# Performance work log

Hardware: AMD Instinct MI355X
Metric: run time of the kernel (lower is better)

## Reference

```python
import jax, jax.numpy as jnp
import numpy as np

INPUT_SIZE = 1024
HIDDEN_SIZE = 1024
N_LAYERS = 2
OUTPUT_SIZE = 4096
BATCH = 4096


def setup_inputs() -> dict:
    key = jax.random.key(0)
    ks = jax.random.split(key, 12)
    s = 1.0 / np.sqrt(HIDDEN_SIZE)
    u = lambda k, shp: jax.random.uniform(k, shp, jnp.float32, -s, s)
    return {
        "input": jax.random.normal(ks[0], (1, BATCH, INPUT_SIZE), jnp.float32),
        "hidden": jax.random.normal(ks[1], (N_LAYERS, BATCH, HIDDEN_SIZE), jnp.float32),
        # nn.RNN layer 0 params
        "W_ih0": u(ks[2], (HIDDEN_SIZE, INPUT_SIZE)),
        "W_hh0": u(ks[3], (HIDDEN_SIZE, HIDDEN_SIZE)),
        "b_ih0": u(ks[4], (HIDDEN_SIZE,)),
        "b_hh0": u(ks[5], (HIDDEN_SIZE,)),
        # nn.RNN layer 1 params (input is layer-0 hidden)
        "W_ih1": u(ks[6], (HIDDEN_SIZE, HIDDEN_SIZE)),
        "W_hh1": u(ks[7], (HIDDEN_SIZE, HIDDEN_SIZE)),
        "b_ih1": u(ks[8], (HIDDEN_SIZE,)),
        "b_hh1": u(ks[9], (HIDDEN_SIZE,)),
        # i2o Linear(input_size + hidden_size, output_size)
        "W_out": u(ks[10], (OUTPUT_SIZE, INPUT_SIZE + HIDDEN_SIZE)),
        "b_out": u(ks[11], (OUTPUT_SIZE,)),
    }


def reference(input, hidden, W_ih0, W_hh0, b_ih0, b_hh0,
              W_ih1, W_hh1, b_ih1, b_hh1, W_out, b_out):
    x = input[0]  # [B, input_size] (seq_len == 1)
    # nn.RNN single step, tanh nonlinearity, 2 layers
    h0 = jnp.tanh(x @ W_ih0.T + b_ih0 + hidden[0] @ W_hh0.T + b_hh0)   # [B, H]
    h1 = jnp.tanh(h0 @ W_ih1.T + b_ih1 + hidden[1] @ W_hh1.T + b_hh1)  # [B, H]
    new_hidden = jnp.stack([h0, h1], axis=0)  # [n_layers, B, H]
    # combined = cat(input[0], hidden[0]) where hidden is the NEW hidden
    combined = jnp.concatenate([x, h0], axis=1)  # [B, input+hidden]
    logits = combined @ W_out.T + b_out          # [B, output_size]
    out = jax.nn.log_softmax(logits, axis=1)
    return (out, new_hidden)
```

## Files before the change

kernel.cpp:

```cpp
#include <hip/hip_runtime.h>
#include <math.h>


typedef __attribute__((ext_vector_type(8))) short bf16x8;
typedef __attribute__((ext_vector_type(4))) float f32x4;

__device__ __forceinline__ unsigned short f2b_rne(float f) {
    unsigned int x = __float_as_uint(f);
    x += 0x7FFF + ((x >> 16) & 1);
    return (unsigned short)(x >> 16);
}

__device__ __forceinline__ void gload_lds16(const void* g, void* l) {
    __builtin_amdgcn_global_load_lds(
        (const __attribute__((address_space(1))) void*)g,
        (__attribute__((address_space(3))) void*)l,
        16, 0, 0);
}

struct CvtSeg { const float* src; unsigned short* dst; unsigned n8; };
struct CvtArgs { CvtSeg seg[8]; };

__global__ __launch_bounds__(256) void f2b_multi(CvtArgs a)
{
    unsigned i = blockIdx.x * 256u + threadIdx.x;
#pragma unroll
    for (int s = 0; s < 8; ++s) {
        if (i < a.seg[s].n8) {
            const float4* src = (const float4*)a.seg[s].src;
            float4 u = src[2 * (size_t)i];
            float4 v = src[2 * (size_t)i + 1];
            unsigned short t[8] = {
                f2b_rne(u.x), f2b_rne(u.y), f2b_rne(u.z), f2b_rne(u.w),
                f2b_rne(v.x), f2b_rne(v.y), f2b_rne(v.z), f2b_rne(v.w)};
            *(uint4*)(a.seg[s].dst + 8 * (size_t)i) = *(const uint4*)t;
            return;
        }
        i -= a.seg[s].n8;
    }
}

struct GemmP {
    const unsigned short *Aa, *Ab; int lda;
    const unsigned short *Wa, *Wb; int ldw;
    const float *ba, *bb;
    float* C; int ldc;
    unsigned short* Cb; int ldcb;
    int nx, nb, do_tanh;
};

template<int BM, int BN>
__device__ __forceinline__ void gemm2p_body(
    const GemmP& p, int bid0, unsigned short* As, unsigned short* Ws, int tid)
{
    constexpr int FM = BM / 32;
    constexpr int FN = BN / 32;
    int bid = (bid0 & 7) * (p.nb >> 3) + (bid0 >> 3);
    const int row0 = (bid / p.nx) * BM;
    const int col0 = (bid % p.nx) * BN;

    const int wid = tid >> 6, lane = tid & 63;
    const int wr = wid >> 1, wc = wid & 1;
    const int fr = lane & 15, fk = lane >> 4;

    f32x4 acc[FM][FN] = {};

    for (int h = 0; h < 2; ++h) {
        const unsigned short* A = h ? p.Ab : p.Aa;
        const unsigned short* W = h ? p.Wb : p.Wa;
        for (int k0 = 0; k0 < 1024; k0 += 32) {
#pragma unroll
            for (int i = 0; i < BM / 64; ++i) {
                int c = i * 256 + wid * 64 + lane;
                int r = c >> 2, ol = c & 3;
                int os = ol ^ ((r >> 1) & 3);
                gload_lds16(A + (size_t)(row0 + r) * p.lda + k0 + os * 8,
                            As + (i * 256 + wid * 64) * 8);
            }
#pragma unroll
            for (int i = 0; i < BN / 64; ++i) {
                int c = i * 256 + wid * 64 + lane;
                int r = c >> 2, ol = c & 3;
                int os = ol ^ ((r >> 1) & 3);
                gload_lds16(W + (size_t)(col0 + r) * p.ldw + k0 + os * 8,
                            Ws + (i * 256 + wid * 64) * 8);
            }
            __syncthreads();

            bf16x8 af[FM], wf[FN];
#pragma unroll
            for (int m = 0; m < FM; ++m) {
                int r = wr * (BM / 2) + m * 16 + fr;
                af[m] = *(const bf16x8*)&As[r * 32 + ((fk ^ ((r >> 1) & 3)) * 8)];
            }
#pragma unroll
            for (int n = 0; n < FN; ++n) {
                int r = wc * (BN / 2) + n * 16 + fr;
                wf[n] = *(const bf16x8*)&Ws[r * 32 + ((fk ^ ((r >> 1) & 3)) * 8)];
            }
#pragma unroll
            for (int m = 0; m < FM; ++m)
#pragma unroll
                for (int n = 0; n < FN; ++n)
                    acc[m][n] = __builtin_amdgcn_mfma_f32_16x16x32_bf16(
                        af[m], wf[n], acc[m][n], 0, 0, 0);
            __syncthreads();
        }
    }

    const bool dot = p.do_tanh != 0;
#pragma unroll
    for (int n = 0; n < FN; ++n) {
        const int col = col0 + wc * (BN / 2) + n * 16 + fr;
        float b = p.ba[col];
        if (p.bb) b += p.bb[col];
#pragma unroll
        for (int m = 0; m < FM; ++m) {
#pragma unroll
            for (int j = 0; j < 4; ++j) {
                const int r = row0 + wr * (BM / 2) + m * 16 + fk * 4 + j;
                float v = acc[m][n][j] + b;
                if (dot) v = tanhf(v);
                p.C[(size_t)r * p.ldc + col] = v;
                if (p.Cb) p.Cb[(size_t)r * p.ldcb + col] = f2b_rne(v);
            }
        }
    }
}

__global__ __launch_bounds__(256) void gemm1_k(GemmP p)
{
    __shared__ __align__(16) unsigned short As[128 * 32];
    __shared__ __align__(16) unsigned short Ws[64 * 32];
    gemm2p_body<128, 64>(p, blockIdx.x, As, Ws, threadIdx.x);
}

__device__ __forceinline__ void logsoftmax_row(float* __restrict__ p, int tid)
{
    const int lane = tid & 63;
    const int wv = tid >> 6;
    __shared__ float redm[4];
    __shared__ float reds[4];

    float v[16];
#pragma unroll
    for (int i = 0; i < 16; ++i) v[i] = p[tid + i * 256];

    float m = v[0];
#pragma unroll
    for (int i = 1; i < 16; ++i) m = fmaxf(m, v[i]);
#pragma unroll
    for (int off = 32; off; off >>= 1) m = fmaxf(m, __shfl_xor(m, off));
    if (lane == 0) redm[wv] = m;
    __syncthreads();
    m = fmaxf(fmaxf(redm[0], redm[1]), fmaxf(redm[2], redm[3]));

    float s = 0.f;
#pragma unroll
    for (int i = 0; i < 16; ++i) s += expf(v[i] - m);
#pragma unroll
    for (int off = 32; off; off >>= 1) s += __shfl_xor(s, off);
    if (lane == 0) reds[wv] = s;
    __syncthreads();
    s = reds[0] + reds[1] + reds[2] + reds[3];

    const float lse = m + logf(s);
#pragma unroll
    for (int i = 0; i < 16; ++i) p[tid + i * 256] = v[i] - lse;
}

__global__ __launch_bounds__(256) void g2sm_k(GemmP p, float* __restrict__ logits)
{
    if (blockIdx.x < 512) {
        __shared__ __align__(16) unsigned short As[128 * 32];
        __shared__ __align__(16) unsigned short Ws[64 * 32];
        gemm2p_body<128, 64>(p, blockIdx.x, As, Ws, threadIdx.x);
    } else {
        logsoftmax_row(logits + (size_t)(blockIdx.x - 512) * 4096, threadIdx.x);
    }
}


__device__ __forceinline__ void stage_half8(
    const unsigned short* __restrict__ src, int ld, int base_rc, int tau, int h,
    unsigned short* lds, int wid, int lane, bool isA)
{
    unsigned short* dst = lds + (tau & 1) * 16384 + h * 8192 + wid * 1024;
    const int k0 = (tau & 15) << 6;
#pragma unroll
    for (int i = 0; i < 2; ++i) {
        int c = wid * 128 + i * 64 + lane;
        int ir = c >> 3, cc = c & 7;
        int grow = isA ? (base_rc + h * 64 + (ir & 63) + ((ir >> 6) << 7))
                       : (base_rc + h * 32 + (ir & 31) + ((ir >> 5) << 6));
        int gk = k0 + (((cc ^ ir) & 7) << 3);
        gload_lds16(src + (size_t)grow * ld + gk, dst + i * 512);
    }
}

__global__ __launch_bounds__(512, 2) void gemm8p(
    const unsigned short* __restrict__ Aa, const unsigned short* __restrict__ Ab,
    const unsigned short* __restrict__ Wa, const unsigned short* __restrict__ Wb,
    int lda, int ldw, const float* __restrict__ bias,
    float* __restrict__ C, int ldc, int nx)
{
    constexpr int NT = 32;
    __shared__ __align__(16) unsigned short smem[65536];
    unsigned short* As = smem;
    unsigned short* Bs = smem + 32768;

    int bid = blockIdx.x;
    bid = (bid & 7) * 32 + (bid >> 3);
    const int row0 = (bid / nx) * 256;
    const int col0 = (bid % nx) * 256;

    const int tid = threadIdx.x;
    const int wid = tid >> 6, lane = tid & 63;
    const int wr = wid >> 2, wc = wid & 3;
    const int fr = lane & 15, fk = lane >> 4;
    const int ch0 = fk ^ (fr & 7);
    const int ch1 = ch0 ^ 4;

#define STA8(tau, h) stage_half8(((tau) < 16 ? Aa : Ab), lda, row0, (tau), (h), As, wid, lane, true)
#define STB8(tau, h) stage_half8(((tau) < 16 ? Wa : Wb), ldw, col0, (tau), (h), Bs, wid, lane, false)

#define LDAF(QM) { const unsigned short* Ap_ = Abase + (QM) * 8192;           \
    _Pragma("unroll") for (int mf = 0; mf < 4; ++mf) {                        \
        int ia = wr * 64 + mf * 16 + fr;                                      \
        af[mf][0] = *(const bf16x8*)&Ap_[ia * 64 + ch0 * 8];                  \
        af[mf][1] = *(const bf16x8*)&Ap_[ia * 64 + ch1 * 8]; } }

#define LDWF(QN, WF) { const unsigned short* Bp_ = Bbase + (QN) * 8192;       \
    _Pragma("unroll") for (int nf = 0; nf < 2; ++nf) {                        \
        int ib = wc * 32 + nf * 16 + fr;                                      \
        WF[nf][0] = *(const bf16x8*)&Bp_[ib * 64 + ch0 * 8];                  \
        WF[nf][1] = *(const bf16x8*)&Bp_[ib * 64 + ch1 * 8]; } }

#define MMQ(QM, QN, WF) {                                                     \
    __builtin_amdgcn_s_setprio(1);                                            \
    _Pragma("unroll") for (int mf = 0; mf < 4; ++mf)                          \
    _Pragma("unroll") for (int nf = 0; nf < 2; ++nf) {                        \
        acc[QM][QN][mf][nf] = __builtin_amdgcn_mfma_f32_16x16x32_bf16(        \
            af[mf][0], WF[nf][0], acc[QM][QN][mf][nf], 0, 0, 0);              \
        acc[QM][QN][mf][nf] = __builtin_amdgcn_mfma_f32_16x16x32_bf16(        \
            af[mf][1], WF[nf][1], acc[QM][QN][mf][nf], 0, 0, 0); }            \
    __builtin_amdgcn_s_setprio(0); }

    f32x4 acc[2][2][4][2] = {};
    bf16x8 af[4][2], wfA[2][2], wfB[2][2];

    STA8(0, 0); STB8(0, 0); STB8(0, 1); STA8(0, 1);

    for (int t = 0; t < NT; ++t) {
        const unsigned short* Abase = As + (t & 1) * 16384;
        const unsigned short* Bbase = Bs + (t & 1) * 16384;
        const bool more = (t + 1 < NT);

        asm volatile("s_waitcnt vmcnt(4)" ::: "memory");
        __builtin_amdgcn_s_barrier();
        LDAF(0); LDWF(0, wfA);
        if (more) STA8(t + 1, 0);
        MMQ(0, 0, wfA);

        if (more) { asm volatile("s_waitcnt vmcnt(4)" ::: "memory"); }
        else      { asm volatile("s_waitcnt vmcnt(2)" ::: "memory"); }
        __builtin_amdgcn_s_barrier();
        LDWF(1, wfB);
        if (more) STB8(t + 1, 0);
        MMQ(0, 1, wfB);

        if (more) { asm volatile("s_waitcnt vmcnt(4)" ::: "memory"); }
        else      { asm volatile("s_waitcnt vmcnt(0)" ::: "memory"); }
        __builtin_amdgcn_s_barrier();
        LDAF(1);
        if (more) STB8(t + 1, 1);
        MMQ(1, 1, wfB);

        if (more) STA8(t + 1, 1);
        MMQ(1, 0, wfA);
    }
#undef MMQ
#undef LDAF
#undef LDWF
#undef STA8
#undef STB8

    float bv[2][2];
#pragma unroll
    for (int qn = 0; qn < 2; ++qn)
#pragma unroll
        for (int nf = 0; nf < 2; ++nf)
            bv[qn][nf] = bias[col0 + wc * 64 + qn * 32 + nf * 16 + fr];

    float* Ct = (float*)smem;
    __syncthreads();
#pragma unroll
    for (int qm = 0; qm < 2; ++qm) {
        if (qm) __syncthreads();
#pragma unroll
        for (int qn = 0; qn < 2; ++qn)
#pragma unroll
            for (int nf = 0; nf < 2; ++nf) {
                const int col = wc * 64 + qn * 32 + nf * 16 + fr;
#pragma unroll
                for (int mf = 0; mf < 4; ++mf)
#pragma unroll
                    for (int j = 0; j < 4; ++j) {
                        int lr = wr * 64 + mf * 16 + fk * 4 + j;
                        int pc = col ^ (((lr >> 2) & 3) << 4);
                        Ct[lr * 256 + pc] = acc[qm][qn][mf][nf][j] + bv[qn][nf];
                    }
            }
        __syncthreads();
#pragma unroll
        for (int k = 0; k < 16; ++k) {
            int idx = k * 512 + tid;
            int lrow = idx >> 6, c4 = idx & 63;
            int pc4 = (c4 * 4) ^ (((lrow >> 2) & 3) << 4);
            int grow = row0 + qm * 64 + (lrow & 63) + ((lrow >> 6) << 7);
            *(float4*)&C[(size_t)grow * ldc + col0 + c4 * 4] =
                *(const float4*)&Ct[lrow * 256 + pc4];
        }
    }
}

extern "C" void kernel_launch(void* const* d_in, const int* in_sizes, int n_in,
                              void* d_out, int out_size, void* d_ws, size_t ws_size,
                              hipStream_t stream)
{
    (void)in_sizes; (void)n_in; (void)out_size; (void)ws_size;

    const float* input  = (const float*)d_in[0];
    const float* hidden = (const float*)d_in[1];
    const float* b_ih0  = (const float*)d_in[4];
    const float* b_hh0  = (const float*)d_in[5];
    const float* b_ih1  = (const float*)d_in[8];
    const float* b_hh1  = (const float*)d_in[9];
    const float* b_out  = (const float*)d_in[11];

    float* out = (float*)d_out;
    float* h0  = out + (size_t)4096 * 4096;
    float* h1  = h0 + (size_t)4096 * 1024;

    unsigned short* xb    = (unsigned short*)d_ws;
    unsigned short* hidb  = xb    + (size_t)4096 * 1024;
    unsigned short* h0b   = hidb  + (size_t)2 * 4096 * 1024;
    unsigned short* Wih0b = h0b   + (size_t)4096 * 1024;
    unsigned short* Whh0b = Wih0b + (size_t)1024 * 1024;
    unsigned short* Wih1b = Whh0b + (size_t)1024 * 1024;
    unsigned short* Whh1b = Wih1b + (size_t)1024 * 1024;
    unsigned short* Woutb = Whh1b + (size_t)1024 * 1024;
    unsigned short* hid0b = hidb;
    unsigned short* hid1b = hidb + (size_t)4096 * 1024;

    CvtArgs ca;
    ca.seg[0] = { input,                 xb,    524288u };
    ca.seg[1] = { hidden,                hidb, 1048576u };
    ca.seg[2] = { (const float*)d_in[2], Wih0b, 131072u };
    ca.seg[3] = { (const float*)d_in[3], Whh0b, 131072u };
    ca.seg[4] = { (const float*)d_in[6], Wih1b, 131072u };
    ca.seg[5] = { (const float*)d_in[7], Whh1b, 131072u };
    ca.seg[6] = { (const float*)d_in[10],Woutb, 1048576u };
    ca.seg[7] = { nullptr, nullptr, 0u };
    hipLaunchKernelGGL(f2b_multi, dim3(12288), dim3(256), 0, stream, ca);

    GemmP p1;
    p1.Aa = xb;    p1.Ab = hid0b; p1.lda = 1024;
    p1.Wa = Wih0b; p1.Wb = Whh0b; p1.ldw = 1024;
    p1.ba = b_ih0; p1.bb = b_hh0;
    p1.C = h0; p1.ldc = 1024; p1.Cb = h0b; p1.ldcb = 1024;
    p1.nx = 16; p1.nb = 512; p1.do_tanh = 1;
    hipLaunchKernelGGL(gemm1_k, dim3(512), dim3(256), 0, stream, p1);

    hipLaunchKernelGGL(gemm8p, dim3(256), dim3(512), 0, stream,
                       xb, h0b, Woutb, Woutb + 1024, 1024, 2048,
                       b_out, out, 4096, 16);

    GemmP p2;
    p2.Aa = h0b;   p2.Ab = hid1b; p2.lda = 1024;
    p2.Wa = Wih1b; p2.Wb = Whh1b; p2.ldw = 1024;
    p2.ba = b_ih1; p2.bb = b_hh1;
    p2.C = h1; p2.ldc = 1024; p2.Cb = nullptr; p2.ldcb = 0;
    p2.nx = 16; p2.nb = 512; p2.do_tanh = 1;
    hipLaunchKernelGGL(g2sm_k, dim3(4608), dim3(256), 0, stream, p2, out);
}
```

Baseline: 170.5 us.

## Vectorize log-softmax row access and restructure GEMM barrier/waitcnt schedule

The log-softmax row routine now loads and stores with float4 instead of scalar strided accesses, so each thread touches contiguous 16-byte chunks. The 8-wave GEMM main loop gains extra barriers with lgkmcnt(0) waits after each LDS fragment read and global-to-LDS stage issue, ahead of the MFMA block. The waitcnt+barrier at the top of each iteration moves to the end, with a prologue barrier added. This aims to synchronize waves around the MFMA clusters, ping-pong style, so memory issue and math from different waves interleave. It also adds more barriers per iteration, which can cost stall time.

Measured after the change: 172.8 us. Within noise of the previous version (+1.3%).

```diff
diff --git a/kernel.cpp b/kernel.cpp
--- a/kernel.cpp
+++ b/kernel.cpp
@@ -142,13 +142,15 @@
     __shared__ float redm[4];
     __shared__ float reds[4];
 
-    float v[16];
-#pragma unroll
-    for (int i = 0; i < 16; ++i) v[i] = p[tid + i * 256];
-
-    float m = v[0];
-#pragma unroll
-    for (int i = 1; i < 16; ++i) m = fmaxf(m, v[i]);
+    float4 v[4];
+#pragma unroll
+    for (int i = 0; i < 4; ++i) v[i] = ((const float4*)p)[i * 256 + tid];
+
+    float m = v[0].x;
+#pragma unroll
+    for (int i = 0; i < 4; ++i) {
+        m = fmaxf(m, fmaxf(fmaxf(v[i].x, v[i].y), fmaxf(v[i].z, v[i].w)));
+    }
 #pragma unroll
     for (int off = 32; off; off >>= 1) m = fmaxf(m, __shfl_xor(m, off));
     if (lane == 0) redm[wv] = m;
@@ -157,7 +159,10 @@
 
     float s = 0.f;
 #pragma unroll
-    for (int i = 0; i < 16; ++i) s += expf(v[i] - m);
+    for (int i = 0; i < 4; ++i) {
+        s += expf(v[i].x - m); s += expf(v[i].y - m);
+        s += expf(v[i].z - m); s += expf(v[i].w - m);
+    }
 #pragma unroll
     for (int off = 32; off; off >>= 1) s += __shfl_xor(s, off);
     if (lane == 0) reds[wv] = s;
@@ -166,7 +171,12 @@
 
     const float lse = m + logf(s);
 #pragma unroll
-    for (int i = 0; i < 16; ++i) p[tid + i * 256] = v[i] - lse;
+    for (int i = 0; i < 4; ++i) {
+        float4 o;
+        o.x = v[i].x - lse; o.y = v[i].y - lse;
+        o.z = v[i].z - lse; o.w = v[i].w - lse;
+        ((float4*)p)[i * 256 + tid] = o;
+    }
 }
 
 __global__ __launch_bounds__(256) void g2sm_k(GemmP p, float* __restrict__ logits)
@@ -246,44 +256,54 @@
             af[mf][1], WF[nf][1], acc[QM][QN][mf][nf], 0, 0, 0); }            \
     __builtin_amdgcn_s_setprio(0); }
 
+#define BAR() __builtin_amdgcn_s_barrier()
+#define LGKM0() asm volatile("s_waitcnt lgkmcnt(0)" ::: "memory")
+
     f32x4 acc[2][2][4][2] = {};
     bf16x8 af[4][2], wfA[2][2], wfB[2][2];
 
     STA8(0, 0); STB8(0, 0); STB8(0, 1); STA8(0, 1);
+    asm volatile("s_waitcnt vmcnt(4)" ::: "memory");
+    BAR();
 
     for (int t = 0; t < NT; ++t) {
         const unsigned short* Abase = As + (t & 1) * 16384;
         const unsigned short* Bbase = Bs + (t & 1) * 16384;
         const bool more = (t + 1 < NT);
 
-        asm volatile("s_waitcnt vmcnt(4)" ::: "memory");
-        __builtin_amdgcn_s_barrier();
         LDAF(0); LDWF(0, wfA);
         if (more) STA8(t + 1, 0);
+        BAR(); LGKM0();
         MMQ(0, 0, wfA);
-
         if (more) { asm volatile("s_waitcnt vmcnt(4)" ::: "memory"); }
         else      { asm volatile("s_waitcnt vmcnt(2)" ::: "memory"); }
-        __builtin_amdgcn_s_barrier();
+        BAR();
+
         LDWF(1, wfB);
         if (more) STB8(t + 1, 0);
+        BAR(); LGKM0();
         MMQ(0, 1, wfB);
-
         if (more) { asm volatile("s_waitcnt vmcnt(4)" ::: "memory"); }
         else      { asm volatile("s_waitcnt vmcnt(0)" ::: "memory"); }
-        __builtin_amdgcn_s_barrier();
+        BAR();
+
         LDAF(1);
         if (more) STB8(t + 1, 1);
+        BAR(); LGKM0();
         MMQ(1, 1, wfB);
 
         if (more) STA8(t + 1, 1);
         MMQ(1, 0, wfA);
+        if (more) asm volatile("s_waitcnt vmcnt(4)" ::: "memory");
+        BAR();
     }
 #undef MMQ
 #undef LDAF
 #undef LDWF
 #undef STA8
 #undef STB8
+#undef BAR
+#undef LGKM0
 
     float bv[2][2];
 #pragma unroll
```

## Store intermediate logits as bf16 and vectorize log-softmax loads

Applied to the files above, without the earlier changes.

The output GEMM now writes its logits as bf16 into a workspace buffer instead of fp32 into the output. The log-softmax pass reads these bf16 values and writes the final fp32 result, which cuts the traffic of the logits round trip. The fallback fp32 log-softmax path is rewritten to use float4 loads and stores. Storing logits in bf16 lowers their precision before the softmax, and the new path only runs when the workspace is large enough.

New measurement: 170.7 us. Within noise of the previous version (+0.1%).

```diff
diff --git a/kernel.cpp b/kernel.cpp
--- a/kernel.cpp
+++ b/kernel.cpp
@@ -135,20 +135,21 @@
     gemm2p_body<128, 64>(p, blockIdx.x, As, Ws, threadIdx.x);
 }
 
-__device__ __forceinline__ void logsoftmax_row(float* __restrict__ p, int tid)
+__device__ __forceinline__ void logsoftmax_row_f32(float* __restrict__ p, int tid)
 {
     const int lane = tid & 63;
     const int wv = tid >> 6;
     __shared__ float redm[4];
     __shared__ float reds[4];
 
-    float v[16];
-#pragma unroll
-    for (int i = 0; i < 16; ++i) v[i] = p[tid + i * 256];
-
-    float m = v[0];
-#pragma unroll
-    for (int i = 1; i < 16; ++i) m = fmaxf(m, v[i]);
+    float4 v[4];
+#pragma unroll
+    for (int i = 0; i < 4; ++i) v[i] = ((const float4*)p)[i * 256 + tid];
+
+    float m = v[0].x;
+#pragma unroll
+    for (int i = 0; i < 4; ++i)
+        m = fmaxf(m, fmaxf(fmaxf(v[i].x, v[i].y), fmaxf(v[i].z, v[i].w)));
 #pragma unroll
     for (int off = 32; off; off >>= 1) m = fmaxf(m, __shfl_xor(m, off));
     if (lane == 0) redm[wv] = m;
@@ -157,7 +158,10 @@
 
     float s = 0.f;
 #pragma unroll
-    for (int i = 0; i < 16; ++i) s += expf(v[i] - m);
+    for (int i = 0; i < 4; ++i) {
+        s += expf(v[i].x - m); s += expf(v[i].y - m);
+        s += expf(v[i].z - m); s += expf(v[i].w - m);
+    }
 #pragma unroll
     for (int off = 32; off; off >>= 1) s += __shfl_xor(s, off);
     if (lane == 0) reds[wv] = s;
@@ -166,17 +170,79 @@
 
     const float lse = m + logf(s);
 #pragma unroll
-    for (int i = 0; i < 16; ++i) p[tid + i * 256] = v[i] - lse;
-}
-
-__global__ __launch_bounds__(256) void g2sm_k(GemmP p, float* __restrict__ logits)
+    for (int i = 0; i < 4; ++i) {
+        float4 o;
+        o.x = v[i].x - lse; o.y = v[i].y - lse;
+        o.z = v[i].z - lse; o.w = v[i].w - lse;
+        ((float4*)p)[i * 256 + tid] = o;
+    }
+}
+
+__device__ __forceinline__ void logsoftmax_row_b16(
+    const unsigned short* __restrict__ lb, float* __restrict__ op, int tid)
+{
+    const int lane = tid & 63;
+    const int wv = tid >> 6;
+    __shared__ float redm[4];
+    __shared__ float reds[4];
+
+    uint4 r[2];
+    r[0] = *(const uint4*)&lb[tid * 8];
+    r[1] = *(const uint4*)&lb[2048 + tid * 8];
+    float v[16];
+#pragma unroll
+    for (int h = 0; h < 2; ++h)
+#pragma unroll
+        for (int j = 0; j < 4; ++j) {
+            unsigned u = ((const unsigned*)&r[h])[j];
+            v[h * 8 + 2 * j]     = __uint_as_float(u << 16);
+            v[h * 8 + 2 * j + 1] = __uint_as_float(u & 0xFFFF0000u);
+        }
+
+    float m = v[0];
+#pragma unroll
+    for (int i = 1; i < 16; ++i) m = fmaxf(m, v[i]);
+#pragma unroll
+    for (int off = 32; off; off >>= 1) m = fmaxf(m, __shfl_xor(m, off));
+    if (lane == 0) redm[wv] = m;
+    __syncthreads();
+    m = fmaxf(fmaxf(redm[0], redm[1]), fmaxf(redm[2], redm[3]));
+
+    float s = 0.f;
+#pragma unroll
+    for (int i = 0; i < 16; ++i) s += expf(v[i] - m);
+#pragma unroll
+    for (int off = 32; off; off >>= 1) s += __shfl_xor(s, off);
+    if (lane == 0) reds[wv] = s;
+    __syncthreads();
+    s = reds[0] + reds[1] + reds[2] + reds[3];
+
+    const float lse = m + logf(s);
+#pragma unroll
+    for (int h = 0; h < 2; ++h) {
+        float4 o0, o1;
+        o0.x = v[h*8+0]-lse; o0.y = v[h*8+1]-lse; o0.z = v[h*8+2]-lse; o0.w = v[h*8+3]-lse;
+        o1.x = v[h*8+4]-lse; o1.y = v[h*8+5]-lse; o1.z = v[h*8+6]-lse; o1.w = v[h*8+7]-lse;
+        *(float4*)&op[h * 2048 + tid * 8]     = o0;
+        *(float4*)&op[h * 2048 + tid * 8 + 4] = o1;
+    }
+}
+
+template<bool B16>
+__global__ __launch_bounds__(256) void g2sm_k(
+    GemmP p, float* __restrict__ out, const unsigned short* __restrict__ lb16)
 {
     if (blockIdx.x < 512) {
         __shared__ __align__(16) unsigned short As[128 * 32];
         __shared__ __align__(16) unsigned short Ws[64 * 32];
         gemm2p_body<128, 64>(p, blockIdx.x, As, Ws, threadIdx.x);
     } else {
-        logsoftmax_row(logits + (size_t)(blockIdx.x - 512) * 4096, threadIdx.x);
+        const int row = blockIdx.x - 512;
+        if (B16)
+            logsoftmax_row_b16(lb16 + (size_t)row * 4096,
+                               out + (size_t)row * 4096, threadIdx.x);
+        else
+            logsoftmax_row_f32(out + (size_t)row * 4096, threadIdx.x);
     }
 }
 
@@ -198,11 +264,12 @@
     }
 }
 
+template<bool B16OUT>
 __global__ __launch_bounds__(512, 2) void gemm8p(
     const unsigned short* __restrict__ Aa, const unsigned short* __restrict__ Ab,
     const unsigned short* __restrict__ Wa, const unsigned short* __restrict__ Wb,
     int lda, int ldw, const float* __restrict__ bias,
-    float* __restrict__ C, int ldc, int nx)
+    float* __restrict__ C, unsigned short* __restrict__ Cb16, int ldc, int nx)
 {
     constexpr int NT = 32;
     __shared__ __align__(16) unsigned short smem[65536];
@@ -318,8 +385,15 @@
             int lrow = idx >> 6, c4 = idx & 63;
             int pc4 = (c4 * 4) ^ (((lrow >> 2) & 3) << 4);
             int grow = row0 + qm * 64 + (lrow & 63) + ((lrow >> 6) << 7);
-            *(float4*)&C[(size_t)grow * ldc + col0 + c4 * 4] =
-                *(const float4*)&Ct[lrow * 256 + pc4];
+            float4 v = *(const float4*)&Ct[lrow * 256 + pc4];
+            if (B16OUT) {
+                unsigned short o[4] = { f2b_rne(v.x), f2b_rne(v.y),
+                                        f2b_rne(v.z), f2b_rne(v.w) };
+                *(ushort4*)&Cb16[(size_t)grow * ldc + col0 + c4 * 4] =
+                    *(const ushort4*)o;
+            } else {
+                *(float4*)&C[(size_t)grow * ldc + col0 + c4 * 4] = v;
+            }
         }
     }
 }
@@ -328,7 +402,7 @@
                               void* d_out, int out_size, void* d_ws, size_t ws_size,
                               hipStream_t stream)
 {
-    (void)in_sizes; (void)n_in; (void)out_size; (void)ws_size;
+    (void)in_sizes; (void)n_in; (void)out_size;
 
     const float* input  = (const float*)d_in[0];
     const float* hidden = (const float*)d_in[1];
@@ -350,8 +424,11 @@
     unsigned short* Wih1b = Whh0b + (size_t)1024 * 1024;
     unsigned short* Whh1b = Wih1b + (size_t)1024 * 1024;
     unsigned short* Woutb = Whh1b + (size_t)1024 * 1024;
+    unsigned short* lb16  = Woutb + (size_t)4096 * 2048;
     unsigned short* hid0b = hidb;
     unsigned short* hid1b = hidb + (size_t)4096 * 1024;
+
+    const bool useB16 = ws_size >= 92274688ull;
 
     CvtArgs ca;
     ca.seg[0] = { input,                 xb,    524288u };
@@ -372,9 +449,15 @@
     p1.nx = 16; p1.nb = 512; p1.do_tanh = 1;
     hipLaunchKernelGGL(gemm1_k, dim3(512), dim3(256), 0, stream, p1);
 
-    hipLaunchKernelGGL(gemm8p, dim3(256), dim3(512), 0, stream,
-                       xb, h0b, Woutb, Woutb + 1024, 1024, 2048,
-                       b_out, out, 4096, 16);
+    if (useB16) {
+        hipLaunchKernelGGL((gemm8p<true>), dim3(256), dim3(512), 0, stream,
+                           xb, h0b, Woutb, Woutb + 1024, 1024, 2048,
+                           b_out, out, lb16, 4096, 16);
+    } else {
+        hipLaunchKernelGGL((gemm8p<false>), dim3(256), dim3(512), 0, stream,
+                           xb, h0b, Woutb, Woutb + 1024, 1024, 2048,
+                           b_out, out, lb16, 4096, 16);
+    }
 
     GemmP p2;
     p2.Aa = h0b;   p2.Ab = hid1b; p2.lda = 1024;
@@ -382,5 +465,11 @@
     p2.ba = b_ih1; p2.bb = b_hh1;
     p2.C = h1; p2.ldc = 1024; p2.Cb = nullptr; p2.ldcb = 0;
     p2.nx = 16; p2.nb = 512; p2.do_tanh = 1;
-    hipLaunchKernelGGL(g2sm_k, dim3(4608), dim3(256), 0, stream, p2, out);
-}
+    if (useB16) {
+        hipLaunchKernelGGL((g2sm_k<true>), dim3(4608), dim3(256), 0, stream,
+                           p2, out, lb16);
+    } else {
+        hipLaunchKernelGGL((g2sm_k<false>), dim3(4608), dim3(256), 0, stream,
+                           p2, out, lb16);
+    }
+}
```

## Store output logits as bf16 scratch and deepen small GEMM K-tile to 64

Applied to the files above, without the earlier changes.

The big output GEMM now writes logits as bf16 to a workspace buffer instead of fp32 into the output. The log-softmax stage reads those bf16 values with vector loads and writes fp32 results with float4 stores, which cuts the logits round-trip traffic roughly in half. Separately, the two smaller RNN GEMMs double the K-step to 64, using a new XOR swizzle and two MFMAs per fragment pair, so there are half as many barriers per K. Rounding the logits to bf16 before the softmax loses precision.

Measured after the change: 160.7 us, median of 2. -5.7%, faster.

```diff
diff --git a/kernel.cpp b/kernel.cpp
--- a/kernel.cpp
+++ b/kernel.cpp
@@ -68,42 +68,49 @@
     for (int h = 0; h < 2; ++h) {
         const unsigned short* A = h ? p.Ab : p.Aa;
         const unsigned short* W = h ? p.Wb : p.Wa;
-        for (int k0 = 0; k0 < 1024; k0 += 32) {
-#pragma unroll
-            for (int i = 0; i < BM / 64; ++i) {
+        for (int k0 = 0; k0 < 1024; k0 += 64) {
+#pragma unroll
+            for (int i = 0; i < BM / 32; ++i) {
                 int c = i * 256 + wid * 64 + lane;
-                int r = c >> 2, ol = c & 3;
-                int os = ol ^ ((r >> 1) & 3);
-                gload_lds16(A + (size_t)(row0 + r) * p.lda + k0 + os * 8,
+                int r = c >> 3, cc = c & 7;
+                int gk = k0 + (((cc ^ r) & 7) << 3);
+                gload_lds16(A + (size_t)(row0 + r) * p.lda + gk,
                             As + (i * 256 + wid * 64) * 8);
             }
 #pragma unroll
-            for (int i = 0; i < BN / 64; ++i) {
+            for (int i = 0; i < BN / 32; ++i) {
                 int c = i * 256 + wid * 64 + lane;
-                int r = c >> 2, ol = c & 3;
-                int os = ol ^ ((r >> 1) & 3);
-                gload_lds16(W + (size_t)(col0 + r) * p.ldw + k0 + os * 8,
+                int r = c >> 3, cc = c & 7;
+                int gk = k0 + (((cc ^ r) & 7) << 3);
+                gload_lds16(W + (size_t)(col0 + r) * p.ldw + gk,
                             Ws + (i * 256 + wid * 64) * 8);
             }
             __syncthreads();
 
-            bf16x8 af[FM], wf[FN];
+            bf16x8 af[FM][2], wf[FN][2];
 #pragma unroll
             for (int m = 0; m < FM; ++m) {
                 int r = wr * (BM / 2) + m * 16 + fr;
-                af[m] = *(const bf16x8*)&As[r * 32 + ((fk ^ ((r >> 1) & 3)) * 8)];
+                int cc = fk ^ (r & 7);
+                af[m][0] = *(const bf16x8*)&As[r * 64 + cc * 8];
+                af[m][1] = *(const bf16x8*)&As[r * 64 + (cc ^ 4) * 8];
             }
 #pragma unroll
             for (int n = 0; n < FN; ++n) {
                 int r = wc * (BN / 2) + n * 16 + fr;
-                wf[n] = *(const bf16x8*)&Ws[r * 32 + ((fk ^ ((r >> 1) & 3)) * 8)];
+                int cc = fk ^ (r & 7);
+                wf[n][0] = *(const bf16x8*)&Ws[r * 64 + cc * 8];
+                wf[n][1] = *(const bf16x8*)&Ws[r * 64 + (cc ^ 4) * 8];
             }
 #pragma unroll
             for (int m = 0; m < FM; ++m)
 #pragma unroll
-                for (int n = 0; n < FN; ++n)
+                for (int n = 0; n < FN; ++n) {
                     acc[m][n] = __builtin_amdgcn_mfma_f32_16x16x32_bf16(
-                        af[m], wf[n], acc[m][n], 0, 0, 0);
+                        af[m][0], wf[n][0], acc[m][n], 0, 0, 0);
+                    acc[m][n] = __builtin_amdgcn_mfma_f32_16x16x32_bf16(
+                        af[m][1], wf[n][1], acc[m][n], 0, 0, 0);
+                }
             __syncthreads();
         }
     }
@@ -130,21 +137,31 @@
 
 __global__ __launch_bounds__(256) void gemm1_k(GemmP p)
 {
-    __shared__ __align__(16) unsigned short As[128 * 32];
-    __shared__ __align__(16) unsigned short Ws[64 * 32];
+    __shared__ __align__(16) unsigned short As[128 * 64];
+    __shared__ __align__(16) unsigned short Ws[64 * 64];
     gemm2p_body<128, 64>(p, blockIdx.x, As, Ws, threadIdx.x);
 }
 
-__device__ __forceinline__ void logsoftmax_row(float* __restrict__ p, int tid)
+__device__ __forceinline__ void logsoftmax_row_b16(
+    const unsigned short* __restrict__ lb, float* __restrict__ op, int tid)
 {
     const int lane = tid & 63;
     const int wv = tid >> 6;
     __shared__ float redm[4];
     __shared__ float reds[4];
 
+    uint4 r[2];
+    r[0] = *(const uint4*)&lb[tid * 8];
+    r[1] = *(const uint4*)&lb[2048 + tid * 8];
     float v[16];
 #pragma unroll
-    for (int i = 0; i < 16; ++i) v[i] = p[tid + i * 256];
+    for (int h = 0; h < 2; ++h)
+#pragma unroll
+        for (int j = 0; j < 4; ++j) {
+            unsigned u = ((const unsigned*)&r[h])[j];
+            v[h * 8 + 2 * j]     = __uint_as_float(u << 16);
+            v[h * 8 + 2 * j + 1] = __uint_as_float(u & 0xFFFF0000u);
+        }
 
     float m = v[0];
 #pragma unroll
@@ -166,17 +183,26 @@
 
     const float lse = m + logf(s);
 #pragma unroll
-    for (int i = 0; i < 16; ++i) p[tid + i * 256] = v[i] - lse;
-}
-
-__global__ __launch_bounds__(256) void g2sm_k(GemmP p, float* __restrict__ logits)
+    for (int h = 0; h < 2; ++h) {
+        float4 o0, o1;
+        o0.x = v[h*8+0]-lse; o0.y = v[h*8+1]-lse; o0.z = v[h*8+2]-lse; o0.w = v[h*8+3]-lse;
+        o1.x = v[h*8+4]-lse; o1.y = v[h*8+5]-lse; o1.z = v[h*8+6]-lse; o1.w = v[h*8+7]-lse;
+        *(float4*)&op[h * 2048 + tid * 8]     = o0;
+        *(float4*)&op[h * 2048 + tid * 8 + 4] = o1;
+    }
+}
+
+__global__ __launch_bounds__(256) void g2sm_k(
+    GemmP p, float* __restrict__ out, const unsigned short* __restrict__ lb16)
 {
     if (blockIdx.x < 512) {
-        __shared__ __align__(16) unsigned short As[128 * 32];
-        __shared__ __align__(16) unsigned short Ws[64 * 32];
+        __shared__ __align__(16) unsigned short As[128 * 64];
+        __shared__ __align__(16) unsigned short Ws[64 * 64];
         gemm2p_body<128, 64>(p, blockIdx.x, As, Ws, threadIdx.x);
     } else {
-        logsoftmax_row(logits + (size_t)(blockIdx.x - 512) * 4096, threadIdx.x);
+        const int row = blockIdx.x - 512;
+        logsoftmax_row_b16(lb16 + (size_t)row * 4096,
+                           out + (size_t)row * 4096, threadIdx.x);
     }
 }
 
@@ -202,7 +228,7 @@
     const unsigned short* __restrict__ Aa, const unsigned short* __restrict__ Ab,
     const unsigned short* __restrict__ Wa, const unsigned short* __restrict__ Wb,
     int lda, int ldw, const float* __restrict__ bias,
-    float* __restrict__ C, int ldc, int nx)
+    unsigned short* __restrict__ Cb16, int ldc, int nx)
 {
     constexpr int NT = 32;
     __shared__ __align__(16) unsigned short smem[65536];
@@ -318,8 +344,11 @@
             int lrow = idx >> 6, c4 = idx & 63;
             int pc4 = (c4 * 4) ^ (((lrow >> 2) & 3) << 4);
             int grow = row0 + qm * 64 + (lrow & 63) + ((lrow >> 6) << 7);
-            *(float4*)&C[(size_t)grow * ldc + col0 + c4 * 4] =
-                *(const float4*)&Ct[lrow * 256 + pc4];
+            float4 v = *(const float4*)&Ct[lrow * 256 + pc4];
+            unsigned short o[4] = { f2b_rne(v.x), f2b_rne(v.y),
+                                    f2b_rne(v.z), f2b_rne(v.w) };
+            *(ushort4*)&Cb16[(size_t)grow * ldc + col0 + c4 * 4] =
+                *(const ushort4*)o;
         }
     }
 }
@@ -350,6 +379,7 @@
     unsigned short* Wih1b = Whh0b + (size_t)1024 * 1024;
     unsigned short* Whh1b = Wih1b + (size_t)1024 * 1024;
     unsigned short* Woutb = Whh1b + (size_t)1024 * 1024;
+    unsigned short* lb16  = Woutb + (size_t)4096 * 2048;
     unsigned short* hid0b = hidb;
     unsigned short* hid1b = hidb + (size_t)4096 * 1024;
 
@@ -374,7 +404,7 @@
 
     hipLaunchKernelGGL(gemm8p, dim3(256), dim3(512), 0, stream,
                        xb, h0b, Woutb, Woutb + 1024, 1024, 2048,
-                       b_out, out, 4096, 16);
+                       b_out, lb16, 4096, 16);
 
     GemmP p2;
     p2.Aa = h0b;   p2.Ab = hid1b; p2.lda = 1024;
@@ -382,5 +412,5 @@
     p2.ba = b_ih1; p2.bb = b_hh1;
     p2.C = h1; p2.ldc = 1024; p2.Cb = nullptr; p2.ldcb = 0;
     p2.nx = 16; p2.nb = 512; p2.do_tanh = 1;
-    hipLaunchKernelGGL(g2sm_k, dim3(4608), dim3(256), 0, stream, p2, out);
-}
+    hipLaunchKernelGGL(g2sm_k, dim3(4608), dim3(256), 0, stream, p2, out, lb16);
+}
```
